# Kernel optimization log

Measured on AMD Instinct MI355X. Metric: run time of the kernel, lower is better.

The kernel has to match this reference:

```python
import jax, jax.numpy as jnp
import numpy as np

N = 80000   # active voxels
G = 64      # voxel grid side
K = 27      # 3x3x3 kernel taps


def _build_coord_maps():
    """Random unique voxel coords in a G^3 grid; 27-tap neighbor index map (-1 = missing)."""
    rng = np.random.default_rng(0)
    flat = rng.choice(G ** 3, size=N, replace=False).astype(np.int64)
    coords = np.stack(np.unravel_index(flat, (G, G, G)), axis=1)  # (N,3)
    order = np.argsort(flat)
    skeys = flat[order]
    offs = [(dx, dy, dz) for dx in (-1, 0, 1) for dy in (-1, 0, 1) for dz in (-1, 0, 1)]
    nbr = np.full((K, N), -1, np.int32)
    for k, (dx, dy, dz) in enumerate(offs):
        nc = coords + np.array([dx, dy, dz])
        inb = np.all((nc >= 0) & (nc < G), axis=1)
        nkey = nc[:, 0] * G * G + nc[:, 1] * G + nc[:, 2]
        pos = np.clip(np.searchsorted(skeys, nkey), 0, N - 1)
        hit = inb & (skeys[pos] == nkey)
        nbr[k] = np.where(hit, order[pos], -1)
    return nbr


_W_SPECS = [('a1w', (27, 96, 64)), ('a2w', (64, 64)), ('a3w', (27, 64, 64)), ('a4w', (64, 64)),
            ('b1w', (27, 256, 64)), ('b2w', (64, 64)), ('b3w', (27, 64, 32)), ('b4w', (32, 32)),
            ('c1w', (27, 96, 128)), ('c2w', (128, 128)), ('c3w', (128, 128))]
_BN_SPECS = [('a1', 64), ('a2', 64), ('a3', 64), ('a4', 64),
             ('b1', 64), ('b2', 64), ('b3', 32), ('b4', 32),
             ('c1', 128), ('c2', 128), ('c3', 128)]


def setup_inputs() -> dict:
    key = jax.random.key(0)
    ks = jax.random.split(key, 64)
    inp = {
        'feat3d': jax.random.normal(ks[0], (N, 96), jnp.float32),
        'feat2d': jax.random.normal(ks[1], (N, 256), jnp.float32),
    }
    i = 2
    for name, shp in _W_SPECS:
        fan = float(np.prod(shp[:-1]))
        inp[name] = jax.random.normal(ks[i], shp, jnp.float32) * (1.0 / np.sqrt(fan))
        i += 1
    for pre, c in _BN_SPECS:  # folded eval-mode BN: y = x*scale + shift
        inp[pre + 's'] = 1.0 + 0.1 * jax.random.normal(ks[i], (c,), jnp.float32)
        inp[pre + 'b'] = 0.1 * jax.random.normal(ks[i + 1], (c,), jnp.float32)
        i += 2
    inp['nbr_idx'] = jnp.asarray(_build_coord_maps())
    inp['align_idx'] = jnp.arange(N, dtype=jnp.int32)  # 2D/3D share coordinates -> exact match
    return inp


def _sconv(x, W, nbr):
    """Sparse 3x3x3 conv: per-tap masked gather + GEMM, accumulated (gather-GEMM-scatter)."""
    out = jnp.zeros((x.shape[0], W.shape[-1]), x.dtype)
    for k in range(W.shape[0]):
        idx = nbr[k]
        g = jnp.where((idx >= 0)[:, None], x[jnp.maximum(idx, 0)], 0.0)
        out = out + g @ W[k]
    return out


def _bnrelu(x, s, b):
    return jax.nn.relu(x * s + b)


def reference(feat3d, feat2d,
              a1w, a2w, a3w, a4w, b1w, b2w, b3w, b4w, c1w, c2w, c3w,
              a1s, a1b, a2s, a2b, a3s, a3b, a4s, a4b,
              b1s, b1b, b2s, b2b, b3s, b3b, b4s, b4b,
              c1s, c1b, c2s, c2b, c3s, c3b,
              nbr_idx, align_idx):
    # 3D branch: 96 -> 64 (dropout = identity in eval)
    x = _bnrelu(_sconv(feat3d, a1w, nbr_idx), a1s, a1b)
    x = _bnrelu(x @ a2w, a2s, a2b)
    x = _bnrelu(_sconv(x, a3w, nbr_idx), a3s, a3b)
    x3 = _bnrelu(x @ a4w, a4s, a4b)
    # 2D branch: 256 -> 32
    y = _bnrelu(_sconv(feat2d, b1w, nbr_idx), b1s, b1b)
    y = _bnrelu(y @ b2w, b2s, b2b)
    y = _bnrelu(_sconv(y, b3w, nbr_idx), b3s, b3b)
    y2 = _bnrelu(y @ b4w, b4s, b4b)
    # features_at_coordinates: exact-match gather at the 3D coords, NaN/Inf -> 0
    ya = y2[align_idx]
    ya = jnp.where(jnp.isfinite(ya), ya, 0.0)
    # fusion: concat 64+32=96 -> 128
    z = jnp.concatenate([x3, ya], axis=1)
    z = _bnrelu(_sconv(z, c1w, nbr_idx), c1s, c1b)
    z = _bnrelu(z @ c2w, c2s, c2b)
    z = _bnrelu(z @ c3w, c3s, c3b)
    return z
```

## Files before the change

### kernel.cpp

```cpp
#include <hip/hip_runtime.h>

typedef __bf16 bf16;
typedef __bf16 bf16x8 __attribute__((ext_vector_type(8)));
typedef __bf16 bf16x4 __attribute__((ext_vector_type(4)));
typedef float  f32x4  __attribute__((ext_vector_type(4)));

__global__ void f2b_kernel(const float* __restrict__ src, bf16* __restrict__ dst, int n4) {
    int i = blockIdx.x * 256 + threadIdx.x;
    if (i >= n4) return;
    float4 v = ((const float4*)src)[i];
    bf16x4 o = { (bf16)v.x, (bf16)v.y, (bf16)v.z, (bf16)v.w };
    ((bf16x4*)dst)[i] = o;
}

__global__ void swz_kernel(const float* __restrict__ W, bf16* __restrict__ Wf,
                           int cin, int cout, int total) {
    int e = blockIdx.x * 256 + threadIdx.x;
    if (e >= total) return;
    int per_tap = cin * cout;
    int tap = e / per_tap;
    int t2  = e - tap * per_tap;
    int ntc = cout >> 4;
    int s   = t2 / (ntc * 512);
    int r3  = t2 - s * (ntc * 512);
    int nt  = r3 >> 9;
    int L   = (r3 & 511) >> 3;
    int j   = r3 & 7;
    int k   = s * 32 + (L >> 4) * 8 + j;
    int col = nt * 16 + (L & 15);
    Wf[e] = (bf16)W[((size_t)tap * cin + k) * cout + col];
}

template<int CIN, int COUT, int TAPS, int KTILE>
__global__ __launch_bounds__(256) void layer_kernel(
    const bf16* __restrict__ X,
    const bf16* __restrict__ Wf,
    const int*  __restrict__ nbr,
    const float* __restrict__ sc, const float* __restrict__ sh,
    bf16* __restrict__ Y, float* __restrict__ Yf,
    int ystride, int yoff, int n)
{
    constexpr int NT   = COUT / 16;
    constexpr int KH   = CIN / KTILE;
    constexpr int KS   = KTILE / 32;
    constexpr int CH   = KTILE / 8;
    constexpr int SREG = KTILE / 32;
    constexpr int AST  = KTILE + 8;
    constexpr int WR   = (COUT >= 64) ? 2 : 1;
    constexpr int WC   = (COUT == 128) ? 4 : 2;
    constexpr int RGRP = 4 / WR;
    constexpr int TOTAL = KH * TAPS;
    constexpr int NBUF = (TOTAL > 1) ? 2 : 1;
    constexpr int IDXN = (TAPS > 1) ? TAPS * 64 : 1;

    __shared__ __align__(16) bf16 As[NBUF][64 * AST];
    __shared__ int idxs[IDXN];

    const int tid  = threadIdx.x;
    const int base = blockIdx.x * 64;
    const int lane = tid & 63;
    const int wv   = tid >> 6;
    const int wrow = wv % RGRP;
    const int wcol = wv / RGRP;
    const int m16  = lane & 15;
    const int quad = lane >> 4;

    if (TAPS > 1) {
        for (int e = tid; e < TAPS * 64; e += 256)
            idxs[e] = nbr[(e >> 6) * n + base + (e & 63)];
        __syncthreads();
    }

    float4 sreg[SREG];
    auto issue_loads = [&](int it) {
        int kh = it / TAPS, t = it - kh * TAPS;
#pragma unroll
        for (int j = 0; j < SREG; ++j) {
            int e = tid + 256 * j;
            int r = e / CH, c = e - r * CH;
            int idx = (TAPS == 1) ? (base + r) : idxs[t * 64 + r];
            float4 val = {0.f, 0.f, 0.f, 0.f};
            if (idx >= 0) val = *(const float4*)(X + (size_t)idx * CIN + kh * KTILE + c * 8);
            sreg[j] = val;
        }
    };
    auto store_lds = [&](int buf) {
#pragma unroll
        for (int j = 0; j < SREG; ++j) {
            int e = tid + 256 * j;
            int r = e / CH, c = e - r * CH;
            *(float4*)(&As[buf][r * AST + c * 8]) = sreg[j];
        }
    };

    f32x4 acc[WR][WC];
#pragma unroll
    for (int r = 0; r < WR; ++r)
#pragma unroll
        for (int c = 0; c < WC; ++c) acc[r][c] = (f32x4){0.f, 0.f, 0.f, 0.f};

    issue_loads(0);
    store_lds(0);

    for (int it = 0; it < TOTAL; ++it) {
        __syncthreads();

        int kh = it / TAPS, t = it - kh * TAPS;
        const bf16* wt = Wf + (size_t)t * (CIN * COUT);
        bf16x8 b[KS][WC];
#pragma unroll
        for (int s = 0; s < KS; ++s)
#pragma unroll
            for (int c = 0; c < WC; ++c)
                b[s][c] = *(const bf16x8*)(wt + ((kh * KS + s) * NT + wcol * WC + c) * 512 + lane * 8);

        if (it + 1 < TOTAL) issue_loads(it + 1);

        const int buf = it & (NBUF - 1);
#pragma unroll
        for (int s = 0; s < KS; ++s) {
            bf16x8 a[WR];
#pragma unroll
            for (int r = 0; r < WR; ++r) {
                int row = (wrow * WR + r) * 16 + m16;
                a[r] = *(const bf16x8*)(&As[buf][row * AST + s * 32 + quad * 8]);
            }
#pragma unroll
            for (int r = 0; r < WR; ++r)
#pragma unroll
                for (int c = 0; c < WC; ++c)
                    acc[r][c] = __builtin_amdgcn_mfma_f32_16x16x32_bf16(a[r], b[s][c], acc[r][c], 0, 0, 0);
        }

        if (it + 1 < TOTAL) store_lds((it + 1) & 1);
    }

#pragma unroll
    for (int c = 0; c < WC; ++c) {
        int col = (wcol * WC + c) * 16 + m16;
        float scale = sc[col], shift = sh[col];
#pragma unroll
        for (int r = 0; r < WR; ++r) {
            int row0 = base + (wrow * WR + r) * 16 + quad * 4;
#pragma unroll
            for (int i = 0; i < 4; ++i) {
                float v = acc[r][c][i] * scale + shift;
                v = v > 0.f ? v : 0.f;
                size_t off = (size_t)(row0 + i) * ystride + yoff + col;
                if (Yf) Yf[off] = v;
                else    Y[off] = (bf16)v;
            }
        }
    }
}

__global__ void concat_kernel(const bf16* __restrict__ y2, const int* __restrict__ align,
                              bf16* __restrict__ z, int n) {
    int e = blockIdx.x * 256 + threadIdx.x;
    if (e >= n * 32) return;
    int i = e >> 5, c = e & 31;
    int a = align[i];
    float v = (float)y2[(size_t)a * 32 + c];
    unsigned u = __builtin_bit_cast(unsigned, v);
    if ((u & 0x7f800000u) == 0x7f800000u) v = 0.f;
    z[(size_t)i * 96 + 64 + c] = (bf16)v;
}

extern "C" void kernel_launch(void* const* d_in, const int* in_sizes, int n_in,
                              void* d_out, int out_size, void* d_ws, size_t ws_size,
                              hipStream_t stream) {
    const float* feat3d = (const float*)d_in[0];
    const float* feat2d = (const float*)d_in[1];
    const float* Wsrc[11];
    for (int i = 0; i < 11; ++i) Wsrc[i] = (const float*)d_in[2 + i];
    const float* bn[22];
    for (int i = 0; i < 22; ++i) bn[i] = (const float*)d_in[13 + i];
    const int* nbr   = (const int*)d_in[35];
    const int* align = (const int*)d_in[36];
    float* out = (float*)d_out;

    const int n = in_sizes[0] / 96;

    char* ws = (char*)d_ws;
    size_t off = 0;
    auto alloc = [&](size_t bytes) -> void* {
        void* p = ws + off;
        off = (off + bytes + 255) & ~(size_t)255;
        return p;
    };
    bf16* F3 = (bf16*)alloc((size_t)n * 96 * 2);
    bf16* F2 = (bf16*)alloc((size_t)n * 256 * 2);
    static const int wt_taps[11] = {27, 1, 27, 1, 27, 1, 27, 1, 27, 1, 1};
    static const int wt_cin[11]  = {96, 64, 64, 64, 256, 64, 64, 32, 96, 128, 128};
    static const int wt_cout[11] = {64, 64, 64, 64, 64, 64, 32, 32, 128, 128, 128};
    bf16* Wf[11];
    for (int i = 0; i < 11; ++i)
        Wf[i] = (bf16*)alloc((size_t)wt_taps[i] * wt_cin[i] * wt_cout[i] * 2);
    bf16* tA = (bf16*)alloc((size_t)n * 64 * 2);
    bf16* tB = (bf16*)alloc((size_t)n * 64 * 2);
    bf16* y2 = (bf16*)alloc((size_t)n * 32 * 2);
    bf16* z  = (bf16*)alloc((size_t)n * 96 * 2);
    bf16* w1 = (bf16*)alloc((size_t)n * 128 * 2);
    bf16* w2 = (bf16*)alloc((size_t)n * 128 * 2);

    f2b_kernel<<<(n * 96 / 4 + 255) / 256, 256, 0, stream>>>(feat3d, F3, n * 96 / 4);
    f2b_kernel<<<(n * 256 / 4 + 255) / 256, 256, 0, stream>>>(feat2d, F2, n * 256 / 4);
    for (int i = 0; i < 11; ++i) {
        int total = wt_taps[i] * wt_cin[i] * wt_cout[i];
        swz_kernel<<<(total + 255) / 256, 256, 0, stream>>>(Wsrc[i], Wf[i], wt_cin[i], wt_cout[i], total);
    }

    const int GB = n / 64;

    layer_kernel<96, 64, 27, 96><<<GB, 256, 0, stream>>>(F3, Wf[0], nbr, bn[0], bn[1], tA, nullptr, 64, 0, n);
    layer_kernel<64, 64, 1, 64 ><<<GB, 256, 0, stream>>>(tA, Wf[1], nullptr, bn[2], bn[3], tB, nullptr, 64, 0, n);
    layer_kernel<64, 64, 27, 64><<<GB, 256, 0, stream>>>(tB, Wf[2], nbr, bn[4], bn[5], tA, nullptr, 64, 0, n);
    layer_kernel<64, 64, 1, 64 ><<<GB, 256, 0, stream>>>(tA, Wf[3], nullptr, bn[6], bn[7], z, nullptr, 96, 0, n);

    layer_kernel<256, 64, 27, 128><<<GB, 256, 0, stream>>>(F2, Wf[4], nbr, bn[8], bn[9], tA, nullptr, 64, 0, n);
    layer_kernel<64, 64, 1, 64   ><<<GB, 256, 0, stream>>>(tA, Wf[5], nullptr, bn[10], bn[11], tB, nullptr, 64, 0, n);
    layer_kernel<64, 32, 27, 64  ><<<GB, 256, 0, stream>>>(tB, Wf[6], nbr, bn[12], bn[13], tA, nullptr, 32, 0, n);
    layer_kernel<32, 32, 1, 32   ><<<GB, 256, 0, stream>>>(tA, Wf[7], nullptr, bn[14], bn[15], y2, nullptr, 32, 0, n);

    concat_kernel<<<(n * 32 + 255) / 256, 256, 0, stream>>>(y2, align, z, n);

    layer_kernel<96, 128, 27, 96><<<GB, 256, 0, stream>>>(z, Wf[8], nbr, bn[16], bn[17], w1, nullptr, 128, 0, n);
    layer_kernel<128, 128, 1, 128><<<GB, 256, 0, stream>>>(w1, Wf[9], nullptr, bn[18], bn[19], w2, nullptr, 128, 0, n);
    layer_kernel<128, 128, 1, 128><<<GB, 256, 0, stream>>>(w2, Wf[10], nullptr, bn[20], bn[21], nullptr, out, 128, 0, n);
}
```

Before: 645.5 us.

## Fuse each sparse conv with its following pointwise linear layers in one kernel

```diff
diff --git a/kernel.cpp b/kernel.cpp
--- a/kernel.cpp
+++ b/kernel.cpp
@@ -31,124 +31,262 @@
     Wf[e] = (bf16)W[((size_t)tap * cin + k) * cout + col];
 }
 
-template<int CIN, int COUT, int TAPS, int KTILE>
+template<int CIN, int C1, int TAPS, int KTILE, int C2, int C3>
 __global__ __launch_bounds__(256) void layer_kernel(
     const bf16* __restrict__ X,
-    const bf16* __restrict__ Wf,
+    const bf16* __restrict__ W1,
+    const bf16* __restrict__ W2,
+    const bf16* __restrict__ W3,
     const int*  __restrict__ nbr,
-    const float* __restrict__ sc, const float* __restrict__ sh,
+    const float* __restrict__ sc1, const float* __restrict__ sh1,
+    const float* __restrict__ sc2, const float* __restrict__ sh2,
+    const float* __restrict__ sc3, const float* __restrict__ sh3,
     bf16* __restrict__ Y, float* __restrict__ Yf,
-    int ystride, int yoff, int n)
+    int ystride, int yoff, int n, int nblocks)
 {
-    constexpr int NT   = COUT / 16;
+    constexpr int NT1  = C1 / 16;
     constexpr int KH   = CIN / KTILE;
     constexpr int KS   = KTILE / 32;
     constexpr int CH   = KTILE / 8;
     constexpr int SREG = KTILE / 32;
     constexpr int AST  = KTILE + 8;
-    constexpr int WR   = (COUT >= 64) ? 2 : 1;
-    constexpr int WC   = (COUT == 128) ? 4 : 2;
-    constexpr int RGRP = 4 / WR;
-    constexpr int TOTAL = KH * TAPS;
-    constexpr int NBUF = (TOTAL > 1) ? 2 : 1;
-    constexpr int IDXN = (TAPS > 1) ? TAPS * 64 : 1;
-
-    __shared__ __align__(16) bf16 As[NBUF][64 * AST];
-    __shared__ int idxs[IDXN];
-
-    const int tid  = threadIdx.x;
-    const int base = blockIdx.x * 64;
-    const int lane = tid & 63;
-    const int wv   = tid >> 6;
-    const int wrow = wv % RGRP;
-    const int wcol = wv / RGRP;
-    const int m16  = lane & 15;
-    const int quad = lane >> 4;
-
-    if (TAPS > 1) {
-        for (int e = tid; e < TAPS * 64; e += 256)
-            idxs[e] = nbr[(e >> 6) * n + base + (e & 63)];
-        __syncthreads();
+    constexpr int WR1  = (C1 >= 64) ? 2 : 1;
+    constexpr int WC1  = (C1 == 128) ? 4 : 2;
+    constexpr int RG1  = 4 / WR1;
+    constexpr int ABUF = 64 * AST;
+    constexpr int ABY  = 2 * ABUF * 2;
+    constexpr int LS1  = C1 + 8;
+    constexpr int LS2  = C2 + 8;
+    constexpr int L1BY = 64 * LS1 * 2;
+    constexpr int L2BY = (C3 > 0) ? 64 * LS2 * 2 : 0;
+    constexpr int SBY  = (ABY > L1BY ? (ABY > L2BY ? ABY : L2BY)
+                                     : (L1BY > L2BY ? L1BY : L2BY));
+
+    __shared__ __align__(16) char smem[SBY];
+    __shared__ int idxs[TAPS * 64];
+    bf16* As = (bf16*)smem;
+
+    const int tid = threadIdx.x;
+
+    {
+    }
+    const int bq  = nblocks >> 3, br = nblocks & 7;
+    const int bx  = blockIdx.x & 7, bs = blockIdx.x >> 3;
+    const int sb  = bx * bq + (bx < br ? bx : br) + bs;
+    const int base = sb * 64;
+
+    const int lane  = tid & 63;
+    const int wv    = tid >> 6;
+    const int m16   = lane & 15;
+    const int quad  = lane >> 4;
+    const int wrow1 = wv % RG1;
+    const int wcol1 = wv / RG1;
+
+    for (int e = tid; e < TAPS * 64; e += 256)
+        idxs[e] = nbr[(e >> 6) * n + base + (e & 63)];
+    __syncthreads();
+
+    int rr[SREG], cof[SREG], lofs[SREG];
+#pragma unroll
+    for (int j = 0; j < SREG; ++j) {
+        int e = tid + 256 * j;
+        rr[j]   = e / CH;
+        int c   = e - rr[j] * CH;
+        cof[j]  = c * 8;
+        lofs[j] = rr[j] * AST + c * 8;
     }
 
     float4 sreg[SREG];
-    auto issue_loads = [&](int it) {
-        int kh = it / TAPS, t = it - kh * TAPS;
+    auto issue_loads = [&](int kh, int t) {
 #pragma unroll
         for (int j = 0; j < SREG; ++j) {
-            int e = tid + 256 * j;
-            int r = e / CH, c = e - r * CH;
-            int idx = (TAPS == 1) ? (base + r) : idxs[t * 64 + r];
+            int idx = idxs[t * 64 + rr[j]];
             float4 val = {0.f, 0.f, 0.f, 0.f};
-            if (idx >= 0) val = *(const float4*)(X + (size_t)idx * CIN + kh * KTILE + c * 8);
+            if (idx >= 0) val = *(const float4*)(X + (size_t)idx * CIN + kh * KTILE + cof[j]);
             sreg[j] = val;
         }
     };
     auto store_lds = [&](int buf) {
 #pragma unroll
-        for (int j = 0; j < SREG; ++j) {
-            int e = tid + 256 * j;
-            int r = e / CH, c = e - r * CH;
-            *(float4*)(&As[buf][r * AST + c * 8]) = sreg[j];
-        }
+        for (int j = 0; j < SREG; ++j)
+            *(float4*)(&As[buf * ABUF + lofs[j]]) = sreg[j];
     };
 
-    f32x4 acc[WR][WC];
-#pragma unroll
-    for (int r = 0; r < WR; ++r)
-#pragma unroll
-        for (int c = 0; c < WC; ++c) acc[r][c] = (f32x4){0.f, 0.f, 0.f, 0.f};
-
-    issue_loads(0);
+    f32x4 acc1[WR1][WC1];
+#pragma unroll
+    for (int r = 0; r < WR1; ++r)
+#pragma unroll
+        for (int c = 0; c < WC1; ++c) acc1[r][c] = (f32x4){0.f, 0.f, 0.f, 0.f};
+
+    issue_loads(0, 0);
     store_lds(0);
 
-    for (int it = 0; it < TOTAL; ++it) {
+    int it = 0;
+    for (int kh = 0; kh < KH; ++kh)
+        for (int t = 0; t < TAPS; ++t, ++it) {
+            __syncthreads();
+
+            const bf16* wt = W1 + (size_t)t * (CIN * C1);
+            bf16x8 bfr[KS][WC1];
+#pragma unroll
+            for (int s = 0; s < KS; ++s)
+#pragma unroll
+                for (int c = 0; c < WC1; ++c)
+                    bfr[s][c] = *(const bf16x8*)(wt + ((kh * KS + s) * NT1 + wcol1 * WC1 + c) * 512 + lane * 8);
+
+            int t2 = t + 1, kh2 = kh;
+            if (t2 == TAPS) { t2 = 0; kh2 = kh + 1; }
+            const bool more = (kh2 < KH);
+            if (more) issue_loads(kh2, t2);
+
+            const int buf = it & 1;
+#pragma unroll
+            for (int s = 0; s < KS; ++s) {
+                bf16x8 a[WR1];
+#pragma unroll
+                for (int r = 0; r < WR1; ++r)
+                    a[r] = *(const bf16x8*)(&As[buf * ABUF + ((wrow1 * WR1 + r) * 16 + m16) * AST + s * 32 + quad * 8]);
+#pragma unroll
+                for (int r = 0; r < WR1; ++r)
+#pragma unroll
+                    for (int c = 0; c < WC1; ++c)
+                        acc1[r][c] = __builtin_amdgcn_mfma_f32_16x16x32_bf16(a[r], bfr[s][c], acc1[r][c], 0, 0, 0);
+            }
+
+            if (more) store_lds(buf ^ 1);
+        }
+
+    __syncthreads();
+    bf16* Lt1 = (bf16*)smem;
+#pragma unroll
+    for (int c = 0; c < WC1; ++c) {
+        int col = (wcol1 * WC1 + c) * 16 + m16;
+        float s1 = sc1[col], h1 = sh1[col];
+#pragma unroll
+        for (int r = 0; r < WR1; ++r) {
+            int row0 = (wrow1 * WR1 + r) * 16 + quad * 4;
+#pragma unroll
+            for (int i = 0; i < 4; ++i) {
+                float v = acc1[r][c][i] * s1 + h1;
+                v = v > 0.f ? v : 0.f;
+                Lt1[(row0 + i) * LS1 + col] = (bf16)v;
+            }
+        }
+    }
+    __syncthreads();
+
+    constexpr int NT2 = C2 / 16;
+    constexpr int WR2 = (C2 >= 64) ? 2 : 1;
+    constexpr int WC2 = (C2 == 128) ? 4 : 2;
+    constexpr int RG2 = 4 / WR2;
+    constexpr int KS2 = C1 / 32;
+    const int wrow2 = wv % RG2, wcol2 = wv / RG2;
+
+    f32x4 acc2[WR2][WC2];
+#pragma unroll
+    for (int r = 0; r < WR2; ++r)
+#pragma unroll
+        for (int c = 0; c < WC2; ++c) acc2[r][c] = (f32x4){0.f, 0.f, 0.f, 0.f};
+
+#pragma unroll
+    for (int s = 0; s < KS2; ++s) {
+        bf16x8 a[WR2], bw[WC2];
+#pragma unroll
+        for (int r = 0; r < WR2; ++r)
+            a[r] = *(const bf16x8*)(&Lt1[((wrow2 * WR2 + r) * 16 + m16) * LS1 + s * 32 + quad * 8]);
+#pragma unroll
+        for (int c = 0; c < WC2; ++c)
+            bw[c] = *(const bf16x8*)(W2 + ((s * NT2 + wcol2 * WC2 + c) * 512 + lane * 8));
+#pragma unroll
+        for (int r = 0; r < WR2; ++r)
+#pragma unroll
+            for (int c = 0; c < WC2; ++c)
+                acc2[r][c] = __builtin_amdgcn_mfma_f32_16x16x32_bf16(a[r], bw[c], acc2[r][c], 0, 0, 0);
+    }
+
+    if constexpr (C3 == 0) {
+#pragma unroll
+        for (int c = 0; c < WC2; ++c) {
+            int col = (wcol2 * WC2 + c) * 16 + m16;
+            float s2 = sc2[col], h2 = sh2[col];
+#pragma unroll
+            for (int r = 0; r < WR2; ++r) {
+                int row0 = base + (wrow2 * WR2 + r) * 16 + quad * 4;
+#pragma unroll
+                for (int i = 0; i < 4; ++i) {
+                    float v = acc2[r][c][i] * s2 + h2;
+                    v = v > 0.f ? v : 0.f;
+                    size_t off = (size_t)(row0 + i) * ystride + yoff + col;
+                    if (Yf) Yf[off] = v;
+                    else    Y[off] = (bf16)v;
+                }
+            }
+        }
+    } else {
         __syncthreads();
-
-        int kh = it / TAPS, t = it - kh * TAPS;
-        const bf16* wt = Wf + (size_t)t * (CIN * COUT);
-        bf16x8 b[KS][WC];
-#pragma unroll
-        for (int s = 0; s < KS; ++s)
-#pragma unroll
-            for (int c = 0; c < WC; ++c)
-                b[s][c] = *(const bf16x8*)(wt + ((kh * KS + s) * NT + wcol * WC + c) * 512 + lane * 8);
-
-        if (it + 1 < TOTAL) issue_loads(it + 1);
-
-        const int buf = it & (NBUF - 1);
-#pragma unroll
-        for (int s = 0; s < KS; ++s) {
-            bf16x8 a[WR];
-#pragma unroll
-            for (int r = 0; r < WR; ++r) {
-                int row = (wrow * WR + r) * 16 + m16;
-                a[r] = *(const bf16x8*)(&As[buf][row * AST + s * 32 + quad * 8]);
-            }
-#pragma unroll
-            for (int r = 0; r < WR; ++r)
-#pragma unroll
-                for (int c = 0; c < WC; ++c)
-                    acc[r][c] = __builtin_amdgcn_mfma_f32_16x16x32_bf16(a[r], b[s][c], acc[r][c], 0, 0, 0);
-        }
-
-        if (it + 1 < TOTAL) store_lds((it + 1) & 1);
-    }
-
-#pragma unroll
-    for (int c = 0; c < WC; ++c) {
-        int col = (wcol * WC + c) * 16 + m16;
-        float scale = sc[col], shift = sh[col];
-#pragma unroll
-        for (int r = 0; r < WR; ++r) {
-            int row0 = base + (wrow * WR + r) * 16 + quad * 4;
-#pragma unroll
-            for (int i = 0; i < 4; ++i) {
-                float v = acc[r][c][i] * scale + shift;
-                v = v > 0.f ? v : 0.f;
-                size_t off = (size_t)(row0 + i) * ystride + yoff + col;
-                if (Yf) Yf[off] = v;
-                else    Y[off] = (bf16)v;
+        bf16* Lt2 = (bf16*)smem;
+#pragma unroll
+        for (int c = 0; c < WC2; ++c) {
+            int col = (wcol2 * WC2 + c) * 16 + m16;
+            float s2 = sc2[col], h2 = sh2[col];
+#pragma unroll
+            for (int r = 0; r < WR2; ++r) {
+                int row0 = (wrow2 * WR2 + r) * 16 + quad * 4;
+#pragma unroll
+                for (int i = 0; i < 4; ++i) {
+                    float v = acc2[r][c][i] * s2 + h2;
+                    v = v > 0.f ? v : 0.f;
+                    Lt2[(row0 + i) * LS2 + col] = (bf16)v;
+                }
+            }
+        }
+        __syncthreads();
+
+        constexpr int C3v = (C3 > 0) ? C3 : 16;
+        constexpr int NT3 = C3v / 16;
+        constexpr int WR3 = (C3v >= 64) ? 2 : 1;
+        constexpr int WC3 = (C3v == 128) ? 4 : 2;
+        constexpr int RG3 = 4 / WR3;
+        constexpr int KS3 = C2 / 32;
+        const int wrow3 = wv % RG3, wcol3 = wv / RG3;
+
+        f32x4 acc3[WR3][WC3];
+#pragma unroll
+        for (int r = 0; r < WR3; ++r)
+#pragma unroll
+            for (int c = 0; c < WC3; ++c) acc3[r][c] = (f32x4){0.f, 0.f, 0.f, 0.f};
+
+#pragma unroll
+        for (int s = 0; s < KS3; ++s) {
+            bf16x8 a[WR3], bw[WC3];
+#pragma unroll
+            for (int r = 0; r < WR3; ++r)
+                a[r] = *(const bf16x8*)(&Lt2[((wrow3 * WR3 + r) * 16 + m16) * LS2 + s * 32 + quad * 8]);
+#pragma unroll
+            for (int c = 0; c < WC3; ++c)
+                bw[c] = *(const bf16x8*)(W3 + ((s * NT3 + wcol3 * WC3 + c) * 512 + lane * 8));
+#pragma unroll
+            for (int r = 0; r < WR3; ++r)
+#pragma unroll
+                for (int c = 0; c < WC3; ++c)
+                    acc3[r][c] = __builtin_amdgcn_mfma_f32_16x16x32_bf16(a[r], bw[c], acc3[r][c], 0, 0, 0);
+        }
+
+#pragma unroll
+        for (int c = 0; c < WC3; ++c) {
+            int col = (wcol3 * WC3 + c) * 16 + m16;
+            float s3 = sc3[col], h3 = sh3[col];
+#pragma unroll
+            for (int r = 0; r < WR3; ++r) {
+                int row0 = base + (wrow3 * WR3 + r) * 16 + quad * 4;
+#pragma unroll
+                for (int i = 0; i < 4; ++i) {
+                    float v = acc3[r][c][i] * s3 + h3;
+                    v = v > 0.f ? v : 0.f;
+                    size_t off = (size_t)(row0 + i) * ystride + yoff + col;
+                    if (Yf) Yf[off] = v;
+                    else    Y[off] = (bf16)v;
+                }
             }
         }
     }
@@ -200,8 +338,6 @@
     bf16* tB = (bf16*)alloc((size_t)n * 64 * 2);
     bf16* y2 = (bf16*)alloc((size_t)n * 32 * 2);
     bf16* z  = (bf16*)alloc((size_t)n * 96 * 2);
-    bf16* w1 = (bf16*)alloc((size_t)n * 128 * 2);
-    bf16* w2 = (bf16*)alloc((size_t)n * 128 * 2);
 
     f2b_kernel<<<(n * 96 / 4 + 255) / 256, 256, 0, stream>>>(feat3d, F3, n * 96 / 4);
     f2b_kernel<<<(n * 256 / 4 + 255) / 256, 256, 0, stream>>>(feat2d, F2, n * 256 / 4);
@@ -212,19 +348,28 @@
 
     const int GB = n / 64;
 
-    layer_kernel<96, 64, 27, 96><<<GB, 256, 0, stream>>>(F3, Wf[0], nbr, bn[0], bn[1], tA, nullptr, 64, 0, n);
-    layer_kernel<64, 64, 1, 64 ><<<GB, 256, 0, stream>>>(tA, Wf[1], nullptr, bn[2], bn[3], tB, nullptr, 64, 0, n);
-    layer_kernel<64, 64, 27, 64><<<GB, 256, 0, stream>>>(tB, Wf[2], nbr, bn[4], bn[5], tA, nullptr, 64, 0, n);
-    layer_kernel<64, 64, 1, 64 ><<<GB, 256, 0, stream>>>(tA, Wf[3], nullptr, bn[6], bn[7], z, nullptr, 96, 0, n);
-
-    layer_kernel<256, 64, 27, 128><<<GB, 256, 0, stream>>>(F2, Wf[4], nbr, bn[8], bn[9], tA, nullptr, 64, 0, n);
-    layer_kernel<64, 64, 1, 64   ><<<GB, 256, 0, stream>>>(tA, Wf[5], nullptr, bn[10], bn[11], tB, nullptr, 64, 0, n);
-    layer_kernel<64, 32, 27, 64  ><<<GB, 256, 0, stream>>>(tB, Wf[6], nbr, bn[12], bn[13], tA, nullptr, 32, 0, n);
-    layer_kernel<32, 32, 1, 32   ><<<GB, 256, 0, stream>>>(tA, Wf[7], nullptr, bn[14], bn[15], y2, nullptr, 32, 0, n);
+    layer_kernel<96, 64, 27, 96, 64, 0><<<GB, 256, 0, stream>>>(
+        F3, Wf[0], Wf[1], nullptr, nbr,
+        bn[0], bn[1], bn[2], bn[3], nullptr, nullptr,
+        tB, nullptr, 64, 0, n, GB);
+    layer_kernel<64, 64, 27, 64, 64, 0><<<GB, 256, 0, stream>>>(
+        tB, Wf[2], Wf[3], nullptr, nbr,
+        bn[4], bn[5], bn[6], bn[7], nullptr, nullptr,
+        z, nullptr, 96, 0, n, GB);
+
+    layer_kernel<256, 64, 27, 128, 64, 0><<<GB, 256, 0, stream>>>(
+        F2, Wf[4], Wf[5], nullptr, nbr,
+        bn[8], bn[9], bn[10], bn[11], nullptr, nullptr,
+        tA, nullptr, 64, 0, n, GB);
+    layer_kernel<64, 32, 27, 64, 32, 0><<<GB, 256, 0, stream>>>(
+        tA, Wf[6], Wf[7], nullptr, nbr,
+        bn[12], bn[13], bn[14], bn[15], nullptr, nullptr,
+        y2, nullptr, 32, 0, n, GB);
 
     concat_kernel<<<(n * 32 + 255) / 256, 256, 0, stream>>>(y2, align, z, n);
 
-    layer_kernel<96, 128, 27, 96><<<GB, 256, 0, stream>>>(z, Wf[8], nbr, bn[16], bn[17], w1, nullptr, 128, 0, n);
-    layer_kernel<128, 128, 1, 128><<<GB, 256, 0, stream>>>(w1, Wf[9], nullptr, bn[18], bn[19], w2, nullptr, 128, 0, n);
-    layer_kernel<128, 128, 1, 128><<<GB, 256, 0, stream>>>(w2, Wf[10], nullptr, bn[20], bn[21], nullptr, out, 128, 0, n);
-}
+    layer_kernel<96, 128, 27, 96, 128, 128><<<GB, 256, 0, stream>>>(
+        z, Wf[8], Wf[9], Wf[10], nbr,
+        bn[16], bn[17], bn[18], bn[19], bn[20], bn[21],
+        nullptr, out, 128, 0, n, GB);
+}
```

Result: faster. 593.9 us (-8.0%).
